# Kernel tuning notes

Measured on AMD Instinct MI355X. Metric: run time of the kernel, lower is better.

The kernel has to match this reference:

```python
import jax, jax.numpy as jnp
import numpy as np

B, C_CONV, C_TRANS, L = 2048, 64, 64, 16
CT = C_CONV + C_TRANS            # 128 input channels
DIM = C_TRANS                    # transformer width (must equal trans_dim)
HEADS, DIM_HEAD = 8, 64          # Attention defaults
INNER = HEADS * DIM_HEAD         # 512
DEPTH, FF_HID = 2, 256           # Block1D -> Transformer defaults
WLEN = 4                         # Attention.lenth (hardcoded in source)
SCALE = DIM_HEAD ** -0.5

# static relative-position indices (16x16) from 4x4 coordinate grid
_cord = np.array([[i, j] for i in range(WLEN) for j in range(WLEN)])
_rel = _cord[:, None, :] - _cord[None, :, :] + WLEN - 1   # values in [0, 6]
_REL0, _REL1 = _rel[..., 0], _rel[..., 1]

def _build_sw_mask():
    h, w, p, shift = HEADS // 2, 2, WLEN, WLEN // 2
    m = np.zeros((h, w, p, p, p, p), dtype=bool)
    s = p - shift
    m[-1, :, :s, :, s:, :] = True
    m[-1, :, s:, :, :s, :] = True
    m[:, -1, :, :s, :, s:] = True
    m[:, -1, :, s:, :, :s] = True
    return jnp.asarray(m.reshape(1, h * w, p * p, p * p))  # (1, heads, 16, 16)

_MASK = _build_sw_mask()

def _ln(x, g, b, eps=1e-5):
    m = x.mean(-1, keepdims=True)
    v = ((x - m) ** 2).mean(-1, keepdims=True)
    return (x - m) / jnp.sqrt(v + eps) * g + b

def _conv1d(x, w, b, pad):
    y = jax.lax.conv_general_dilated(x, w, (1,), [(pad, pad)],
                                     dimension_numbers=('NCH', 'OIH', 'NCH'))
    return y + b[None, :, None]

def _attention(x, qkv_w, qkv_b, proj_w, proj_b, relpos):
    b, n, _ = x.shape
    x = jnp.roll(x, -(n // 2), axis=1)            # SW cyclic shift (never un-rolled, as in source)
    qkv = x @ qkv_w.T + qkv_b                     # (b, n, 3*inner)
    q, k, v = jnp.split(qkv, 3, axis=-1)
    sh = lambda t: t.reshape(b, n, HEADS, DIM_HEAD).transpose(0, 2, 1, 3)
    q, k, v = sh(q), sh(k), sh(v)
    dots = jnp.einsum('bhid,bhjd->bhij', q, k) * SCALE
    dots = dots + relpos[:, _REL0, _REL1][None]   # gathered relative-position bias (heads,n,n)
    dots = jnp.where(_MASK[:, :, :n, :n], -1e9, dots)
    attn = jax.nn.softmax(dots, axis=-1)
    out = jnp.einsum('bhij,bhjd->bhid', attn, v)
    out = out.transpose(0, 2, 1, 3).reshape(b, n, INNER)
    return out @ proj_w.T + proj_b

def _forward(x, c11_w, c11_b, c12_w, c12_b, lse1_w, lse1_b, lse2_w, lse2_b,
             ln1_g, ln1_b, ln2_g, ln2_b, mlp1_w, mlp1_b, mlp2_w, mlp2_b,
             aln_g, aln_b, qkv_w, qkv_b, proj_w, proj_b, relpos,
             fln_g, fln_b, ff1_w, ff1_b, ff2_w, ff2_b):
    y = jax.nn.relu(_conv1d(x, c11_w, c11_b, 0))
    conv_x, trans_x = y[:, :C_CONV], y[:, C_CONV:]
    # LSE residual block, plus the extra residual in VSE.forward
    t = jax.nn.leaky_relu(_conv1d(conv_x, lse1_w, lse1_b, 1), 0.01)
    t = jax.nn.leaky_relu(_conv1d(t, lse2_w, lse2_b, 1), 0.01)
    conv_x = (t + conv_x) + conv_x
    # GSE: Block1D(trans_dim, trans_dim, dim)
    h = trans_x.transpose(0, 2, 1)                # (b, l, c)
    z = _ln(h, ln1_g, ln1_b)
    for i in range(DEPTH):
        z = _attention(_ln(z, aln_g[i], aln_b[i]), qkv_w[i], qkv_b[i],
                       proj_w[i], proj_b[i], relpos[i]) + z
        f = _ln(z, fln_g[i], fln_b[i])
        f = jax.nn.gelu(f @ ff1_w[i].T + ff1_b[i], approximate=False)
        z = f @ ff2_w[i].T + ff2_b[i] + z
    h = h + z                                     # x + msa(ln1(x))
    m = _ln(h, ln2_g, ln2_b)
    m = jax.nn.gelu(m @ mlp1_w.T + mlp1_b, approximate=False)
    h = h + (m @ mlp2_w.T + mlp2_b)               # x + mlp(ln2(x))
    trans_out = h.transpose(0, 2, 1)              # (b, c, l)
    res = _conv1d(jnp.concatenate([conv_x, trans_out], axis=1), c12_w, c12_b, 0)
    return x + res

def setup_inputs() -> dict:
    key = jax.random.key(0)
    ks = iter(jax.random.split(key, 40))
    rnd = lambda shape, s=0.02: jax.random.normal(next(ks), shape, jnp.float32) * s
    return {
        'x': jax.random.normal(next(ks), (B, CT, L), jnp.float32),
        'c11_w': rnd((CT, CT, 1), 0.05), 'c11_b': rnd((CT,)),
        'c12_w': rnd((CT, CT, 1), 0.05), 'c12_b': rnd((CT,)),
        'lse1_w': rnd((C_CONV, C_CONV, 3), 0.05), 'lse1_b': rnd((C_CONV,)),
        'lse2_w': rnd((C_CONV, C_CONV, 3), 0.05), 'lse2_b': rnd((C_CONV,)),
        'ln1_g': jnp.ones((DIM,)), 'ln1_b': jnp.zeros((DIM,)),
        'ln2_g': jnp.ones((DIM,)), 'ln2_b': jnp.zeros((DIM,)),
        'mlp1_w': rnd((4 * DIM, DIM)), 'mlp1_b': rnd((4 * DIM,)),
        'mlp2_w': rnd((DIM, 4 * DIM)), 'mlp2_b': rnd((DIM,)),
        'aln_g': jnp.ones((DEPTH, DIM)), 'aln_b': jnp.zeros((DEPTH, DIM)),
        'qkv_w': rnd((DEPTH, 3 * INNER, DIM)), 'qkv_b': rnd((DEPTH, 3 * INNER)),
        'proj_w': rnd((DEPTH, DIM, INNER)), 'proj_b': rnd((DEPTH, DIM)),
        'relpos': rnd((DEPTH, HEADS, 2 * WLEN - 1, 2 * WLEN - 1)),
        'fln_g': jnp.ones((DEPTH, DIM)), 'fln_b': jnp.zeros((DEPTH, DIM)),
        'ff1_w': rnd((DEPTH, FF_HID, DIM)), 'ff1_b': rnd((DEPTH, FF_HID)),
        'ff2_w': rnd((DEPTH, DIM, FF_HID)), 'ff2_b': rnd((DEPTH, DIM)),
    }

def reference(x, c11_w, c11_b, c12_w, c12_b, lse1_w, lse1_b, lse2_w, lse2_b,
              ln1_g, ln1_b, ln2_g, ln2_b, mlp1_w, mlp1_b, mlp2_w, mlp2_b,
              aln_g, aln_b, qkv_w, qkv_b, proj_w, proj_b, relpos,
              fln_g, fln_b, ff1_w, ff1_b, ff2_w, ff2_b):
    return _forward(x, c11_w, c11_b, c12_w, c12_b, lse1_w, lse1_b, lse2_w, lse2_b,
                    ln1_g, ln1_b, ln2_g, ln2_b, mlp1_w, mlp1_b, mlp2_w, mlp2_b,
                    aln_g, aln_b, qkv_w, qkv_b, proj_w, proj_b, relpos,
                    fln_g, fln_b, ff1_w, ff1_b, ff2_w, ff2_b)
```

## Files before the change

### kernel.cpp

```cpp
#include <hip/hip_runtime.h>
#include <math.h>

#define SA 68
#define SX 132
#define SF 260

__device__ __forceinline__ float lrelu_f(float v){ return v > 0.f ? v : 0.01f*v; }
__device__ __forceinline__ float gelu_f(float v){ return 0.5f*v*(1.f + erff(v*0.70710678118654752f)); }

template<int ND>
__device__ __forceinline__ void gemm_nd(const float* __restrict__ in, int instride, int K,
                                        const float* __restrict__ W, int wstride,
                                        const float* __restrict__ bias,
                                        float* __restrict__ outp, int outstride,
                                        int tid, int act, bool accum)
{
    const int l  = tid & 15;
    const int dq = tid >> 4;
    float acc[ND][4];
#pragma unroll
    for (int nb = 0; nb < ND; ++nb)
#pragma unroll
        for (int dd = 0; dd < 4; ++dd) acc[nb][dd] = 0.f;
    const float* inrow = in + l*instride;
    for (int k = 0; k < K; k += 4) {
        const float4 a4 = *(const float4*)(inrow + k);
#pragma unroll
        for (int nb = 0; nb < ND; ++nb) {
#pragma unroll
            for (int dd = 0; dd < 4; ++dd) {
                const float4 w4 = *(const float4*)(W + (size_t)(nb*64 + dq*4 + dd)*wstride + k);
                acc[nb][dd] += w4.x*a4.x + w4.y*a4.y + w4.z*a4.z + w4.w*a4.w;
            }
        }
    }
#pragma unroll
    for (int nb = 0; nb < ND; ++nb)
#pragma unroll
        for (int dd = 0; dd < 4; ++dd) {
            const int d = nb*64 + dq*4 + dd;
            float v = acc[nb][dd] + (bias ? bias[d] : 0.f);
            if (act == 1) v = v > 0.f ? v : 0.f;
            else if (act == 2) v = gelu_f(v);
            float* o = outp + l*outstride + d;
            if (accum) *o += v; else *o = v;
        }
}

__device__ __forceinline__ void ln16x64(const float* __restrict__ in,
                                        float* __restrict__ outb,
                                        const float* __restrict__ g, const float* __restrict__ bvec,
                                        int tid, bool roll)
{
    const int r = tid >> 4, c0 = (tid & 15) * 4;
    const float4 v = *(const float4*)(in + r*SA + c0);
    float s  = v.x + v.y + v.z + v.w;
    float sq = v.x*v.x + v.y*v.y + v.z*v.z + v.w*v.w;
#pragma unroll
    for (int m = 1; m < 16; m <<= 1) { s += __shfl_xor(s, m, 64); sq += __shfl_xor(sq, m, 64); }
    const float mean = s * (1.f/64.f);
    const float var  = sq * (1.f/64.f) - mean*mean;
    const float rstd = rsqrtf(var + 1e-5f);
    const int rd = roll ? ((r + 8) & 15) : r;
    const float4 gv = *(const float4*)(g + c0);
    const float4 bv = *(const float4*)(bvec + c0);
    float4 o;
    o.x = (v.x-mean)*rstd*gv.x + bv.x;
    o.y = (v.y-mean)*rstd*gv.y + bv.y;
    o.z = (v.z-mean)*rstd*gv.z + bv.z;
    o.w = (v.w-mean)*rstd*gv.w + bv.w;
    *(float4*)(outb + rd*SA + c0) = o;
}

__device__ __forceinline__ void conv3_lrelu(const float* __restrict__ in,
                                            float* __restrict__ outb,
                                            const float* __restrict__ w, const float* __restrict__ bias,
                                            int tid, int mode, float* __restrict__ cxbuf)
{
    const int o = tid >> 2, l0 = (tid & 3) * 4;
    float acc[4] = {0.f, 0.f, 0.f, 0.f};
    const float* wr0 = w + (size_t)o*64*3;
    for (int i = 0; i < 64; ++i) {
        const float* wr = wr0 + i*3;
        const float w0 = wr[0], w1 = wr[1], w2 = wr[2];
        const float* row = in + i*16 + l0;
        const float xm1 = (l0 == 0)  ? 0.f : row[-1];
        const float x0 = row[0], x1 = row[1], x2 = row[2], x3 = row[3];
        const float xp1 = (l0 == 12) ? 0.f : row[4];
        acc[0] += w0*xm1 + w1*x0 + w2*x1;
        acc[1] += w0*x0  + w1*x1 + w2*x2;
        acc[2] += w0*x1  + w1*x2 + w2*x3;
        acc[3] += w0*x2  + w1*x3 + w2*xp1;
    }
    const float bb = bias[o];
    if (mode == 0) {
#pragma unroll
        for (int j = 0; j < 4; ++j) outb[o*16 + l0 + j] = lrelu_f(acc[j] + bb);
    } else {
#pragma unroll
        for (int j = 0; j < 4; ++j) {
            float* p = cxbuf + o*16 + l0 + j;
            *p = lrelu_f(acc[j] + bb) + 2.f * (*p);
        }
    }
}

__global__ __launch_bounds__(256) void vse_fused(
    const float* __restrict__ x,
    const float* __restrict__ c11_w, const float* __restrict__ c11_b,
    const float* __restrict__ c12_w, const float* __restrict__ c12_b,
    const float* __restrict__ lse1_w, const float* __restrict__ lse1_b,
    const float* __restrict__ lse2_w, const float* __restrict__ lse2_b,
    const float* __restrict__ ln1_g, const float* __restrict__ ln1_b,
    const float* __restrict__ ln2_g, const float* __restrict__ ln2_b,
    const float* __restrict__ mlp1_w, const float* __restrict__ mlp1_b,
    const float* __restrict__ mlp2_w, const float* __restrict__ mlp2_b,
    const float* __restrict__ aln_g, const float* __restrict__ aln_b,
    const float* __restrict__ qkv_w, const float* __restrict__ qkv_b,
    const float* __restrict__ proj_w, const float* __restrict__ proj_b,
    const float* __restrict__ relpos,
    const float* __restrict__ fln_g, const float* __restrict__ fln_b,
    const float* __restrict__ ff1_w, const float* __restrict__ ff1_b,
    const float* __restrict__ ff2_w, const float* __restrict__ ff2_b,
    float* __restrict__ out)
{
    __shared__ float s_xt[16*SX];
    __shared__ float s_yt[16*SX];
    __shared__ float s_cx[64*16];
    __shared__ float s_h [16*SA];
    __shared__ float s_z [16*SA];
    __shared__ float s_a [16*SA];
    __shared__ float s_q [16*SA];
    __shared__ float s_k [16*SA];
    __shared__ float s_v [16*SA];
    __shared__ float s_o [16*SA];
    __shared__ float s_po[16*SA];
    __shared__ float s_att[16*16];
    __shared__ float s_f [16*SF];
    float* const s_t1 = s_f;

    const int tid = threadIdx.x;
    const int b = blockIdx.x;
    const float* xb = x + (size_t)b * 2048;

#pragma unroll
    for (int it = 0; it < 8; ++it) {
        const int idx = tid + it*256;
        const int c = idx >> 4, l = idx & 15;
        s_xt[l*SX + c] = xb[idx];
    }
    __syncthreads();

    gemm_nd<2>(s_xt, SX, 128, c11_w, 128, c11_b, s_yt, SX, tid, 1, false);
    __syncthreads();

#pragma unroll
    for (int it = 0; it < 4; ++it) {
        const int idx = tid + it*256;
        const int i = idx & 63, l = idx >> 6;
        s_cx[i*16 + l] = s_yt[l*SX + i];
        s_h [l*SA + i] = s_yt[l*SX + 64 + i];
    }
    __syncthreads();

    conv3_lrelu(s_cx, s_t1, lse1_w, lse1_b, tid, 0, nullptr);
    __syncthreads();
    conv3_lrelu(s_t1, nullptr, lse2_w, lse2_b, tid, 1, s_cx);
    __syncthreads();

    ln16x64(s_h, s_z, ln1_g, ln1_b, tid, false);
    __syncthreads();

    for (int layer = 0; layer < 2; ++layer) {
        const float* qkv_wl = qkv_w + (size_t)layer * 1536 * 64;
        const float* qkv_bl = qkv_b + layer * 1536;
        const float* proj_wl = proj_w + (size_t)layer * 64 * 512;
        const float* proj_bl = proj_b + layer * 64;
        const float* rel_l = relpos + layer * 8 * 49;

        ln16x64(s_z, s_a, aln_g + layer*64, aln_b + layer*64, tid, true);
        __syncthreads();

        for (int hh = 0; hh < 8; ++hh) {
            gemm_nd<1>(s_a, SA, 64, qkv_wl + (size_t)(hh*64)*64,        64, qkv_bl + hh*64,        s_q, SA, tid, 0, false);
            gemm_nd<1>(s_a, SA, 64, qkv_wl + (size_t)(512 + hh*64)*64,  64, qkv_bl + 512 + hh*64,  s_k, SA, tid, 0, false);
            gemm_nd<1>(s_a, SA, 64, qkv_wl + (size_t)(1024 + hh*64)*64, 64, qkv_bl + 1024 + hh*64, s_v, SA, tid, 0, false);
            __syncthreads();

            {
                const int i = tid >> 4, j = tid & 15;
                const float* qi = s_q + i*SA;
                const float* kj = s_k + j*SA;
                float dot = 0.f;
                for (int d0 = 0; d0 < 64; d0 += 4) {
                    const float4 qv = *(const float4*)(qi + d0);
                    const float4 kv = *(const float4*)(kj + d0);
                    dot += qv.x*kv.x + qv.y*kv.y + qv.z*kv.z + qv.w*kv.w;
                }
                float val = dot * 0.125f
                          + rel_l[hh*49 + ((i>>2) - (j>>2) + 3)*7 + ((i&3) - (j&3) + 3)];
                const bool masked = ((hh >= 6) && (((i>>2) < 2) != ((j>>2) < 2)))
                                 || ((hh & 1) && (((i&3) < 2) != ((j&3) < 2)));
                if (masked) val = -1e9f;
                float mx = val;
#pragma unroll
                for (int m = 1; m < 16; m <<= 1) mx = fmaxf(mx, __shfl_xor(mx, m, 64));
                const float e = expf(val - mx);
                float ssum = e;
#pragma unroll
                for (int m = 1; m < 16; m <<= 1) ssum += __shfl_xor(ssum, m, 64);
                s_att[i*16 + j] = e / ssum;
            }
            __syncthreads();

            {
                const int l = tid & 15, dq = tid >> 4;
                float a0 = 0.f, a1 = 0.f, a2 = 0.f, a3 = 0.f;
                for (int j = 0; j < 16; ++j) {
                    const float at = s_att[l*16 + j];
                    const float4 v4 = *(const float4*)(s_v + j*SA + dq*4);
                    a0 += at*v4.x; a1 += at*v4.y; a2 += at*v4.z; a3 += at*v4.w;
                }
                float* op = s_o + l*SA + dq*4;
                op[0] = a0; op[1] = a1; op[2] = a2; op[3] = a3;
            }
            __syncthreads();

            gemm_nd<1>(s_o, SA, 64, proj_wl + hh*64, 512,
                       (hh == 0) ? proj_bl : nullptr, s_po, SA, tid, 0, hh != 0);
            __syncthreads();
        }

#pragma unroll
        for (int it = 0; it < 4; ++it) {
            const int idx = tid + it*256;
            const int d = idx & 63, l = idx >> 6;
            s_z[l*SA + d] += s_po[l*SA + d];
        }
        __syncthreads();

        ln16x64(s_z, s_a, fln_g + layer*64, fln_b + layer*64, tid, false);
        __syncthreads();
        gemm_nd<4>(s_a, SA, 64, ff1_w + (size_t)layer*256*64, 64, ff1_b + layer*256, s_f, SF, tid, 2, false);
        __syncthreads();
        gemm_nd<1>(s_f, SF, 256, ff2_w + (size_t)layer*64*256, 256, ff2_b + layer*64, s_z, SA, tid, 0, true);
        __syncthreads();
    }

#pragma unroll
    for (int it = 0; it < 4; ++it) {
        const int idx = tid + it*256;
        const int d = idx & 63, l = idx >> 6;
        s_h[l*SA + d] += s_z[l*SA + d];
    }
    __syncthreads();
    ln16x64(s_h, s_a, ln2_g, ln2_b, tid, false);
    __syncthreads();
    gemm_nd<4>(s_a, SA, 64, mlp1_w, 64, mlp1_b, s_f, SF, tid, 2, false);
    __syncthreads();
    gemm_nd<1>(s_f, SF, 256, mlp2_w, 256, mlp2_b, s_h, SA, tid, 0, true);
    __syncthreads();

#pragma unroll
    for (int it = 0; it < 8; ++it) {
        const int idx = tid + it*256;
        const int i = idx & 127, l = idx >> 7;
        s_yt[l*SX + i] = (i < 64) ? s_cx[i*16 + l] : s_h[l*SA + (i - 64)];
    }
    __syncthreads();

    gemm_nd<2>(s_yt, SX, 128, c12_w, 128, c12_b, s_f, SF, tid, 0, false);
    __syncthreads();

    float* ob = out + (size_t)b * 2048;
#pragma unroll
    for (int it = 0; it < 8; ++it) {
        const int idx = tid + it*256;
        const int c = idx >> 4, l = idx & 15;
        ob[idx] = s_xt[l*SX + c] + s_f[l*SF + c];
    }
}

extern "C" void kernel_launch(void* const* d_in, const int* in_sizes, int n_in,
                              void* d_out, int out_size, void* d_ws, size_t ws_size,
                              hipStream_t stream)
{
    const float* x      = (const float*)d_in[0];
    const float* c11_w  = (const float*)d_in[1];
    const float* c11_b  = (const float*)d_in[2];
    const float* c12_w  = (const float*)d_in[3];
    const float* c12_b  = (const float*)d_in[4];
    const float* lse1_w = (const float*)d_in[5];
    const float* lse1_b = (const float*)d_in[6];
    const float* lse2_w = (const float*)d_in[7];
    const float* lse2_b = (const float*)d_in[8];
    const float* ln1_g  = (const float*)d_in[9];
    const float* ln1_b  = (const float*)d_in[10];
    const float* ln2_g  = (const float*)d_in[11];
    const float* ln2_b  = (const float*)d_in[12];
    const float* mlp1_w = (const float*)d_in[13];
    const float* mlp1_b = (const float*)d_in[14];
    const float* mlp2_w = (const float*)d_in[15];
    const float* mlp2_b = (const float*)d_in[16];
    const float* aln_g  = (const float*)d_in[17];
    const float* aln_b  = (const float*)d_in[18];
    const float* qkv_w  = (const float*)d_in[19];
    const float* qkv_b  = (const float*)d_in[20];
    const float* proj_w = (const float*)d_in[21];
    const float* proj_b = (const float*)d_in[22];
    const float* relpos = (const float*)d_in[23];
    const float* fln_g  = (const float*)d_in[24];
    const float* fln_b  = (const float*)d_in[25];
    const float* ff1_w  = (const float*)d_in[26];
    const float* ff1_b  = (const float*)d_in[27];
    const float* ff2_w  = (const float*)d_in[28];
    const float* ff2_b  = (const float*)d_in[29];

    const int B = in_sizes[0] / (128 * 16);

    vse_fused<<<dim3(B), dim3(256), 0, stream>>>(
        x, c11_w, c11_b, c12_w, c12_b, lse1_w, lse1_b, lse2_w, lse2_b,
        ln1_g, ln1_b, ln2_g, ln2_b, mlp1_w, mlp1_b, mlp2_w, mlp2_b,
        aln_g, aln_b, qkv_w, qkv_b, proj_w, proj_b, relpos,
        fln_g, fln_b, ff1_w, ff1_b, ff2_w, ff2_b,
        (float*)d_out);
}
```

Before: 1.598 ms.

## Pool and alias shared buffers, template GEMM strides, split FFN for occupancy

Replaces the separate shared arrays with one aliased pool, cutting per-block LDS so more blocks fit per CU, and adds launch bounds asking for 4 blocks. To make this fit, the FFN/MLP hidden layer is computed in two 128-wide halves, and projection output accumulates directly into the residual. The final residual re-reads x from global memory instead of keeping it in LDS. GEMM sizes and strides become template constants with partial unrolling, which may raise register pressure against the new occupancy bound.

```diff
diff --git a/kernel.cpp b/kernel.cpp
--- a/kernel.cpp
+++ b/kernel.cpp
@@ -3,16 +3,15 @@
 
 #define SA 68
 #define SX 132
-#define SF 260
 
 __device__ __forceinline__ float lrelu_f(float v){ return v > 0.f ? v : 0.01f*v; }
 __device__ __forceinline__ float gelu_f(float v){ return 0.5f*v*(1.f + erff(v*0.70710678118654752f)); }
 
-template<int ND>
-__device__ __forceinline__ void gemm_nd(const float* __restrict__ in, int instride, int K,
-                                        const float* __restrict__ W, int wstride,
+template<int ND, int K, int WS, int IS, int OS>
+__device__ __forceinline__ void gemm_nd(const float* __restrict__ in,
+                                        const float* __restrict__ W,
                                         const float* __restrict__ bias,
-                                        float* __restrict__ outp, int outstride,
+                                        float* __restrict__ outp,
                                         int tid, int act, bool accum)
 {
     const int l  = tid & 15;
@@ -22,14 +21,16 @@
     for (int nb = 0; nb < ND; ++nb)
 #pragma unroll
         for (int dd = 0; dd < 4; ++dd) acc[nb][dd] = 0.f;
-    const float* inrow = in + l*instride;
+    const float* inrow = in + l*IS;
+    const float* wbase = W + (size_t)dq*4*WS;
+#pragma unroll 8
     for (int k = 0; k < K; k += 4) {
         const float4 a4 = *(const float4*)(inrow + k);
 #pragma unroll
         for (int nb = 0; nb < ND; ++nb) {
 #pragma unroll
             for (int dd = 0; dd < 4; ++dd) {
-                const float4 w4 = *(const float4*)(W + (size_t)(nb*64 + dq*4 + dd)*wstride + k);
+                const float4 w4 = *(const float4*)(wbase + (size_t)(nb*64 + dd)*WS + k);
                 acc[nb][dd] += w4.x*a4.x + w4.y*a4.y + w4.z*a4.z + w4.w*a4.w;
             }
         }
@@ -42,7 +43,7 @@
             float v = acc[nb][dd] + (bias ? bias[d] : 0.f);
             if (act == 1) v = v > 0.f ? v : 0.f;
             else if (act == 2) v = gelu_f(v);
-            float* o = outp + l*outstride + d;
+            float* o = outp + l*OS + d;
             if (accum) *o += v; else *o = v;
         }
 }
@@ -80,6 +81,7 @@
     const int o = tid >> 2, l0 = (tid & 3) * 4;
     float acc[4] = {0.f, 0.f, 0.f, 0.f};
     const float* wr0 = w + (size_t)o*64*3;
+#pragma unroll 8
     for (int i = 0; i < 64; ++i) {
         const float* wr = wr0 + i*3;
         const float w0 = wr[0], w1 = wr[1], w2 = wr[2];
@@ -105,7 +107,7 @@
     }
 }
 
-__global__ __launch_bounds__(256) void vse_fused(
+__global__ __launch_bounds__(256, 4) void vse_fused(
     const float* __restrict__ x,
     const float* __restrict__ c11_w, const float* __restrict__ c11_b,
     const float* __restrict__ c12_w, const float* __restrict__ c12_b,
@@ -124,20 +126,22 @@
     const float* __restrict__ ff2_w, const float* __restrict__ ff2_b,
     float* __restrict__ out)
 {
-    __shared__ float s_xt[16*SX];
-    __shared__ float s_yt[16*SX];
-    __shared__ float s_cx[64*16];
-    __shared__ float s_h [16*SA];
-    __shared__ float s_z [16*SA];
-    __shared__ float s_a [16*SA];
-    __shared__ float s_q [16*SA];
-    __shared__ float s_k [16*SA];
-    __shared__ float s_v [16*SA];
-    __shared__ float s_o [16*SA];
-    __shared__ float s_po[16*SA];
-    __shared__ float s_att[16*16];
-    __shared__ float s_f [16*SF];
-    float* const s_t1 = s_f;
+    __shared__ float pool[9664];
+    float* const s_h   = pool;
+    float* const s_z   = pool + 1088;
+    float* const s_a   = pool + 2176;
+    float* const s_q   = pool + 3264;
+    float* const s_k   = pool + 4352;
+    float* const s_v   = pool + 5440;
+    float* const s_fh  = pool + 6528;
+    float* const s_cx  = pool + 8640;
+    float* const s_xt  = s_q;
+    float* const s_y   = s_fh;
+    float* const s_t1  = s_a;
+    float* const s_o   = s_fh;
+    float* const s_att = s_fh + 1088;
+    float* const s_cat = s_q;
+    float* const s_res = s_fh;
 
     const int tid = threadIdx.x;
     const int b = blockIdx.x;
@@ -151,15 +155,15 @@
     }
     __syncthreads();
 
-    gemm_nd<2>(s_xt, SX, 128, c11_w, 128, c11_b, s_yt, SX, tid, 1, false);
+    gemm_nd<2,128,128,SX,SX>(s_xt, c11_w, c11_b, s_y, tid, 1, false);
     __syncthreads();
 
 #pragma unroll
     for (int it = 0; it < 4; ++it) {
         const int idx = tid + it*256;
         const int i = idx & 63, l = idx >> 6;
-        s_cx[i*16 + l] = s_yt[l*SX + i];
-        s_h [l*SA + i] = s_yt[l*SX + 64 + i];
+        s_cx[i*16 + l] = s_y[l*SX + i];
+        s_h [l*SA + i] = s_y[l*SX + 64 + i];
     }
     __syncthreads();
 
@@ -172,19 +176,19 @@
     __syncthreads();
 
     for (int layer = 0; layer < 2; ++layer) {
-        const float* qkv_wl = qkv_w + (size_t)layer * 1536 * 64;
-        const float* qkv_bl = qkv_b + layer * 1536;
+        const float* qkv_wl  = qkv_w + (size_t)layer * 1536 * 64;
+        const float* qkv_bl  = qkv_b + layer * 1536;
         const float* proj_wl = proj_w + (size_t)layer * 64 * 512;
         const float* proj_bl = proj_b + layer * 64;
-        const float* rel_l = relpos + layer * 8 * 49;
+        const float* rel_l   = relpos + layer * 8 * 49;
 
         ln16x64(s_z, s_a, aln_g + layer*64, aln_b + layer*64, tid, true);
         __syncthreads();
 
         for (int hh = 0; hh < 8; ++hh) {
-            gemm_nd<1>(s_a, SA, 64, qkv_wl + (size_t)(hh*64)*64,        64, qkv_bl + hh*64,        s_q, SA, tid, 0, false);
-            gemm_nd<1>(s_a, SA, 64, qkv_wl + (size_t)(512 + hh*64)*64,  64, qkv_bl + 512 + hh*64,  s_k, SA, tid, 0, false);
-            gemm_nd<1>(s_a, SA, 64, qkv_wl + (size_t)(1024 + hh*64)*64, 64, qkv_bl + 1024 + hh*64, s_v, SA, tid, 0, false);
+            gemm_nd<1,64,64,SA,SA>(s_a, qkv_wl + (size_t)(hh*64)*64,        qkv_bl + hh*64,        s_q, tid, 0, false);
+            gemm_nd<1,64,64,SA,SA>(s_a, qkv_wl + (size_t)(512 + hh*64)*64,  qkv_bl + 512 + hh*64,  s_k, tid, 0, false);
+            gemm_nd<1,64,64,SA,SA>(s_a, qkv_wl + (size_t)(1024 + hh*64)*64, qkv_bl + 1024 + hh*64, s_v, tid, 0, false);
             __syncthreads();
 
             {
@@ -192,6 +196,7 @@
                 const float* qi = s_q + i*SA;
                 const float* kj = s_k + j*SA;
                 float dot = 0.f;
+#pragma unroll
                 for (int d0 = 0; d0 < 64; d0 += 4) {
                     const float4 qv = *(const float4*)(qi + d0);
                     const float4 kv = *(const float4*)(kj + d0);
@@ -216,6 +221,7 @@
             {
                 const int l = tid & 15, dq = tid >> 4;
                 float a0 = 0.f, a1 = 0.f, a2 = 0.f, a3 = 0.f;
+#pragma unroll
                 for (int j = 0; j < 16; ++j) {
                     const float at = s_att[l*16 + j];
                     const float4 v4 = *(const float4*)(s_v + j*SA + dq*4);
@@ -226,25 +232,22 @@
             }
             __syncthreads();
 
-            gemm_nd<1>(s_o, SA, 64, proj_wl + hh*64, 512,
-                       (hh == 0) ? proj_bl : nullptr, s_po, SA, tid, 0, hh != 0);
-            __syncthreads();
-        }
-
-#pragma unroll
-        for (int it = 0; it < 4; ++it) {
-            const int idx = tid + it*256;
-            const int d = idx & 63, l = idx >> 6;
-            s_z[l*SA + d] += s_po[l*SA + d];
-        }
-        __syncthreads();
+            gemm_nd<1,64,512,SA,SA>(s_o, proj_wl + hh*64,
+                                    (hh == 0) ? proj_bl : nullptr, s_z, tid, 0, true);
+            __syncthreads();
+        }
 
         ln16x64(s_z, s_a, fln_g + layer*64, fln_b + layer*64, tid, false);
         __syncthreads();
-        gemm_nd<4>(s_a, SA, 64, ff1_w + (size_t)layer*256*64, 64, ff1_b + layer*256, s_f, SF, tid, 2, false);
-        __syncthreads();
-        gemm_nd<1>(s_f, SF, 256, ff2_w + (size_t)layer*64*256, 256, ff2_b + layer*64, s_z, SA, tid, 0, true);
-        __syncthreads();
+#pragma unroll
+        for (int p = 0; p < 2; ++p) {
+            gemm_nd<2,64,64,SA,SX>(s_a, ff1_w + (size_t)layer*256*64 + (size_t)p*128*64,
+                                   ff1_b + layer*256 + p*128, s_fh, tid, 2, false);
+            __syncthreads();
+            gemm_nd<1,128,256,SX,SA>(s_fh, ff2_w + (size_t)layer*64*256 + p*128,
+                                     (p == 0) ? (ff2_b + layer*64) : nullptr, s_z, tid, 0, true);
+            __syncthreads();
+        }
     }
 
 #pragma unroll
@@ -256,20 +259,24 @@
     __syncthreads();
     ln16x64(s_h, s_a, ln2_g, ln2_b, tid, false);
     __syncthreads();
-    gemm_nd<4>(s_a, SA, 64, mlp1_w, 64, mlp1_b, s_f, SF, tid, 2, false);
-    __syncthreads();
-    gemm_nd<1>(s_f, SF, 256, mlp2_w, 256, mlp2_b, s_h, SA, tid, 0, true);
-    __syncthreads();
+#pragma unroll
+    for (int p = 0; p < 2; ++p) {
+        gemm_nd<2,64,64,SA,SX>(s_a, mlp1_w + (size_t)p*128*64, mlp1_b + p*128, s_fh, tid, 2, false);
+        __syncthreads();
+        gemm_nd<1,128,256,SX,SA>(s_fh, mlp2_w + p*128,
+                                 (p == 0) ? mlp2_b : nullptr, s_h, tid, 0, true);
+        __syncthreads();
+    }
 
 #pragma unroll
     for (int it = 0; it < 8; ++it) {
         const int idx = tid + it*256;
         const int i = idx & 127, l = idx >> 7;
-        s_yt[l*SX + i] = (i < 64) ? s_cx[i*16 + l] : s_h[l*SA + (i - 64)];
-    }
-    __syncthreads();
-
-    gemm_nd<2>(s_yt, SX, 128, c12_w, 128, c12_b, s_f, SF, tid, 0, false);
+        s_cat[l*SX + i] = (i < 64) ? s_cx[i*16 + l] : s_h[l*SA + (i - 64)];
+    }
+    __syncthreads();
+
+    gemm_nd<2,128,128,SX,SX>(s_cat, c12_w, c12_b, s_res, tid, 0, false);
     __syncthreads();
 
     float* ob = out + (size_t)b * 2048;
@@ -277,7 +284,7 @@
     for (int it = 0; it < 8; ++it) {
         const int idx = tid + it*256;
         const int c = idx >> 4, l = idx & 15;
-        ob[idx] = s_xt[l*SX + c] + s_f[l*SF + c];
+        ob[idx] = xb[idx] + s_res[l*SX + c];
     }
 }
 
```

New measurement: 1.568 ms. Within noise of the previous version (-1.9%).
